# Kernel optimization log

Measured on AMD Instinct MI355X. Metric: run time of the kernel, lower is better.

The kernel has to match this reference:

```python
import jax, jax.numpy as jnp
import numpy as np

B, T, N, F = 4, 12, 768, 32
H, K, KT, L = 64, 2, 3, 2
E = 24576
EPS = 1e-5


def setup_inputs() -> dict:
    key = jax.random.key(0)
    ks = iter(jax.random.split(key, 32))
    nrm = lambda shp, s=0.05: jax.random.normal(next(ks), shp, jnp.float32) * s
    inp = dict(
        x=jax.random.normal(next(ks), (B, T, N, F), jnp.float32),
        edge_index=jax.random.randint(next(ks), (2, E), 0, N),
        edge_weight=jax.random.uniform(next(ks), (E,), jnp.float32),
        in_proj_w=nrm((F, H)), in_proj_b=jnp.zeros((H,), jnp.float32),
        tc_w=nrm((L, 2, 3, H, H, KT)),           # [layer, tconv1/2, P/Q/R, out, in, k]
        tc_b=jnp.zeros((L, 2, 3, H), jnp.float32),
        cheb_w=nrm((L, K, H, H)), cheb_b=jnp.zeros((L, H), jnp.float32),
        bn_g=jnp.ones((L, N), jnp.float32), bn_b=jnp.zeros((L, N), jnp.float32),
        ln_g=jnp.ones((L, H), jnp.float32), ln_b=jnp.zeros((L, H), jnp.float32),
        out1_w=nrm((2 * H, H // 2)), out1_b=jnp.zeros((H // 2,), jnp.float32),
        oln_g=jnp.ones((H // 2,), jnp.float32), oln_b=jnp.zeros((H // 2,), jnp.float32),
        out2_w=nrm((H // 2, 1)), out2_b=jnp.zeros((1,), jnp.float32),
    )
    return inp


def _tconv(x, w, b):
    # gated temporal conv (GLU-style), 'same' padding along T. x: [B,T,N,C]
    xt = x.transpose(0, 3, 2, 1)  # [B,C,N,T]
    pad = (KT - 1) // 2
    def c(i):
        y = jax.lax.conv_general_dilated(
            xt, w[i][:, :, None, :], (1, 1), ((0, 0), (pad, pad)),
            dimension_numbers=('NCHW', 'OIHW', 'NCHW'))
        return y + b[i][None, :, None, None]
    out = jax.nn.relu(c(0) * jax.nn.sigmoid(c(1)) + c(2))
    return out.transpose(0, 3, 2, 1)


def _cheb(x, row, col, lap_w, theta, bias):
    # ChebConv with lambda_max=2: L_hat = -D^-1/2 A D^-1/2. x: [B,T,N,C]
    def lhat(z):
        zn = z.transpose(2, 0, 1, 3)                      # [N,B,T,C]
        msg = zn[col] * lap_w[:, None, None, None]        # gather source nodes
        agg = jax.ops.segment_sum(msg, row, num_segments=N)
        return agg.transpose(1, 2, 0, 3)
    tx0 = x
    out = jnp.einsum('btnc,cd->btnd', tx0, theta[0])
    if K > 1:
        tx1 = lhat(tx0)
        out = out + jnp.einsum('btnc,cd->btnd', tx1, theta[1])
        for k in range(2, K):
            tx2 = 2.0 * lhat(tx1) - tx0
            out = out + jnp.einsum('btnc,cd->btnd', tx2, theta[k])
            tx0, tx1 = tx1, tx2
    return out + bias


def reference(x, edge_index, edge_weight, in_proj_w, in_proj_b, tc_w, tc_b,
              cheb_w, cheb_b, bn_g, bn_b, ln_g, ln_b,
              out1_w, out1_b, oln_g, oln_b, out2_w, out2_b):
    row, col = edge_index[0], edge_index[1]
    deg = jax.ops.segment_sum(edge_weight, row, num_segments=N)
    dinv = jnp.where(deg > 0, jax.lax.rsqrt(jnp.maximum(deg, 1e-12)), 0.0)
    lap_w = -dinv[row] * edge_weight * dinv[col]

    h = x @ in_proj_w + in_proj_b  # [B,T,N,H]
    for l in range(L):
        z = _tconv(h, tc_w[l, 0], tc_b[l, 0])
        z = jax.nn.relu(_cheb(z, row, col, lap_w, cheb_w[l], cheb_b[l]))
        z = _tconv(z, tc_w[l, 1], tc_b[l, 1])
        # BatchNorm2d with nodes as channels: stats over (B,T,C) per node
        mu = z.mean(axis=(0, 1, 3), keepdims=True)
        var = z.var(axis=(0, 1, 3), keepdims=True)
        z = (z - mu) * jax.lax.rsqrt(var + EPS)
        z = z * bn_g[l][None, None, :, None] + bn_b[l][None, None, :, None]
        # LayerNorm over feature dim
        m2 = z.mean(-1, keepdims=True)
        v2 = z.var(-1, keepdims=True)
        z = (z - m2) * jax.lax.rsqrt(v2 + EPS) * ln_g[l] + ln_b[l]
        h = h + z  # dropout = identity (eval)

    emb = h[:, -1]  # [B,N,H] last timestep
    # pairwise linear: cat([row_h, col_h]) @ W == row_h @ W[:H] + col_h @ W[H:]
    a = emb @ out1_w[:H]             # [B,N,H/2]
    c = emb @ out1_w[H:] + out1_b    # [B,N,H/2]
    p = jax.nn.relu(a[:, :, None, :] + c[:, None, :, :])  # [B,N,N,H/2]
    pm = p.mean(-1, keepdims=True)
    pv = p.var(-1, keepdims=True)
    p = (p - pm) * jax.lax.rsqrt(pv + EPS) * oln_g + oln_b
    logits = (p @ out2_w)[..., 0] + out2_b[0]
    return jax.nn.sigmoid(logits)  # [B,N,N]
```

## Files before the change

kernel.cpp:

```cpp
#include <hip/hip_runtime.h>
#include <math.h>

#define NODES 768
#define BB 4
#define TT 12
#define FF 32
#define HH 64
#define EE 24576
#define EPSV 1e-5f

typedef short bf16x8 __attribute__((ext_vector_type(8)));
typedef float f32x4  __attribute__((ext_vector_type(4)));

__device__ __forceinline__ unsigned short f2bf(float f) {
  union { float f; unsigned int u; } c; c.f = f;
  unsigned int u = c.u;
  unsigned int r = (u + 0x7FFFu + ((u >> 16) & 1u)) >> 16;
  return (unsigned short)r;
}

constexpr int OFF_ROWPTR = 1600;
constexpr int OFF_COLS   = 3200;
constexpr int OFF_WSEW   = 27776;
constexpr int OFF_WT     = 52352;
constexpr int OFF_THT    = 199808;
constexpr int OFF_WIN    = 216192;
constexpr int OFF_GW     = 222336;
constexpr int OFF_H      = 222400;
constexpr int OFF_ZA     = 2581696;
constexpr int OFF_ZB     = 4940992;
constexpr int OFF_AGG    = 7300288;
constexpr int OFF_A      = 9661120;
constexpr int OFF_C      = 9759424;

__global__ void prep_kernel(const float* __restrict__ tc_w, const float* __restrict__ cheb_w,
                            const float* __restrict__ in_proj_w, const float* __restrict__ out1_w,
                            const float* __restrict__ oln_g, const float* __restrict__ oln_b,
                            const float* __restrict__ out2_w, float* __restrict__ ws) {
  int idx = blockIdx.x * 256 + threadIdx.x;
  if (idx < 147456) {
    int lj = idx / 36864; int r = idx % 36864;
    int ks = r / 6144;    int r2 = r % 6144;
    int nt = r2 / 512;    int r3 = r2 % 512;
    int l  = r3 >> 3;     int j  = r3 & 7;
    int k  = ks * 32 + ((l >> 4) << 3) + j;
    int kk = k >> 6;      int in = k & 63;
    int col = nt * 16 + (l & 15);
    int g = col >> 6;     int o  = col & 63;
    float v = tc_w[(((lj * 3 + g) * 64 + o) * 64 + in) * 3 + kk];
    ((unsigned short*)(ws + OFF_WT))[idx] = f2bf(v);
  }
  int idx2 = idx - 147456;
  if (idx2 >= 0 && idx2 < 16384) {
    int i = idx2 & 63; int t = idx2 >> 6;
    int o = t & 63; t >>= 6;
    int k = t & 1; int l = t >> 1;
    ws[OFF_THT + idx2] = cheb_w[((l*2 + k)*64 + i)*64 + o];
  }
  int idx3 = idx2 - 16384;
  if (idx3 >= 0 && idx3 < 2048) {
    int i = idx3 & 31; int o = idx3 >> 5;
    ws[OFF_WIN + idx3] = in_proj_w[i*64 + o];
  }
  int idx6 = idx3 - 2048;
  if (idx6 == 0) {
    float S1 = 0.f, S2 = 0.f;
    for (int d = 0; d < 32; d++) {
      float gw = oln_g[d] * out2_w[d];
      ws[OFF_GW + d] = gw;
      S1 += gw;
      S2 += oln_b[d] * out2_w[d];
    }
    ws[OFF_GW + 32] = S1;
    ws[OFF_GW + 33] = S2;
  }
}

__global__ __launch_bounds__(1024) void graph_kernel(const int* __restrict__ ei,
                                                     const float* __restrict__ ew,
                                                     float* __restrict__ ws) {
  __shared__ float sdeg[NODES];
  __shared__ int scnt[NODES];
  __shared__ int soff[NODES];
  __shared__ int sscan[NODES];
  int tid = threadIdx.x;
  if (tid < NODES) { sdeg[tid] = 0.f; scnt[tid] = 0; }
  __syncthreads();
  for (int e = tid; e < EE; e += 1024) {
    int r = ei[e];
    atomicAdd(&sdeg[r], ew[e]);
    atomicAdd(&scnt[r], 1);
  }
  __syncthreads();
  int c = (tid < NODES) ? scnt[tid] : 0;
  if (tid < NODES) sscan[tid] = c;
  __syncthreads();
  for (int d = 1; d < NODES; d <<= 1) {
    int v = 0;
    if (tid < NODES && tid >= d) v = sscan[tid - d];
    __syncthreads();
    if (tid < NODES) sscan[tid] += v;
    __syncthreads();
  }
  if (tid < NODES) {
    soff[tid] = sscan[tid] - c;
    ((int*)ws)[OFF_ROWPTR + tid + 1] = sscan[tid];
    if (tid == 0) ((int*)ws)[OFF_ROWPTR] = 0;
  }
  __syncthreads();
  for (int e = tid; e < EE; e += 1024) {
    int r = ei[e];
    int col = ei[EE + e];
    float w = ew[e];
    float dr = sdeg[r], dc = sdeg[col];
    float dir = dr > 0.f ? rsqrtf(fmaxf(dr, 1e-12f)) : 0.f;
    float dic = dc > 0.f ? rsqrtf(fmaxf(dc, 1e-12f)) : 0.f;
    float lw = -dir * w * dic;
    int pos = atomicAdd(&soff[r], 1);
    ((int*)ws)[OFF_COLS + pos] = col;
    ws[OFF_WSEW + pos] = lw;
  }
}

__global__ __launch_bounds__(64) void inproj_kernel(const float* __restrict__ x,
                                                    const float* __restrict__ in_proj_b,
                                                    float* __restrict__ ws) {
  int bid = blockIdx.x;
  int r0 = (bid >> 2) << 6;
  int o0 = (bid & 3) << 4;
  int row = r0 + threadIdx.x;
  float xr[32];
  const float4* xp = (const float4*)(x + row * 32);
#pragma unroll
  for (int i = 0; i < 8; i++) {
    float4 v = xp[i];
    xr[4*i] = v.x; xr[4*i+1] = v.y; xr[4*i+2] = v.z; xr[4*i+3] = v.w;
  }
  const float* WT = ws + OFF_WIN;
  float* h = ws + OFF_H;
  float4 res[4];
  float* rf = (float*)res;
#pragma unroll
  for (int oo = 0; oo < 16; oo++) {
    int o = o0 + oo;
    float acc = in_proj_b[o];
#pragma unroll
    for (int i = 0; i < 32; i++) acc += xr[i] * WT[o * 32 + i];
    rf[oo] = acc;
  }
  float4* op = (float4*)(h + row * 64 + o0);
#pragma unroll
  for (int q = 0; q < 4; q++) op[q] = res[q];
}

__global__ __launch_bounds__(256) void tconv_kernel(const float* __restrict__ src,
                                                    float* __restrict__ dst,
                                                    const unsigned short* __restrict__ WB,
                                                    const float* __restrict__ bias) {
  __shared__ unsigned short zls[3072];
  __shared__ float cbuf[12 * 192];
  unsigned char* zb = (unsigned char*)zls;
  int tid = threadIdx.x;
  int lane = tid & 63;
  int w = tid >> 6;
  int P0 = blockIdx.x * 3;
  int b  = P0 / NODES;
  int n0 = P0 % NODES;

  bf16x8 bfr[6][3];
#pragma unroll
  for (int ks = 0; ks < 6; ks++) {
#pragma unroll
    for (int c = 0; c < 3; c++) {
      int nt = w * 3 + c;
      bfr[ks][c] = *(const bf16x8*)(WB + (((ks * 12 + nt) * 64 + lane) << 3));
    }
  }
  float B0 = bias[tid & 63];
  float B1 = bias[64 + (tid & 63)];
  float B2 = bias[128 + (tid & 63)];

  for (int e = tid; e < 384; e += 256) {
    int pl = e / 128; int rr = (e >> 6) & 1; int in = e & 63;
    int ts = rr ? 13 : 0;
    int off = pl * 1792 + ts * 128 + ((in * 2) ^ ((ts & 7) << 4));
    *(unsigned short*)(zb + off) = 0;
  }
  for (int e = tid; e < 576; e += 256) {
    int pl = e / 192; int rem = e % 192; int t = rem >> 4; int i4 = rem & 15;
    int c0 = i4 << 2;
    float4 v = *(const float4*)(src + ((b * TT + t) * NODES + n0 + pl) * HH + c0);
    int ts = t + 1;
    int base = pl * 1792 + ts * 128;
    unsigned int lo = ((unsigned int)f2bf(v.y) << 16) | f2bf(v.x);
    unsigned int hi = ((unsigned int)f2bf(v.w) << 16) | f2bf(v.z);
    *(unsigned int*)(zb + (base + (((c0    ) * 2) ^ ((ts & 7) << 4)))) = lo;
    *(unsigned int*)(zb + (base + (((c0 + 2) * 2) ^ ((ts & 7) << 4)))) = hi;
  }
  __syncthreads();

  int tb = (lane >> 4) << 2;
  int cc = lane & 15;
  for (int p = 0; p < 3; p++) {
    bf16x8 afr[6];
#pragma unroll
    for (int ks = 0; ks < 6; ks++) {
      int k0 = ks * 32 + ((lane >> 4) << 3);
      int kk = k0 >> 6; int in0 = k0 & 63;
      int ts = (lane & 15) + kk;
      int off = p * 1792 + ts * 128 + ((in0 * 2) ^ ((ts & 7) << 4));
      afr[ks] = *(const bf16x8*)(zb + off);
    }
    f32x4 a0 = {0.f, 0.f, 0.f, 0.f};
    f32x4 a1 = a0, a2 = a0;
#pragma unroll
    for (int ks = 0; ks < 6; ks++) {
      a0 = __builtin_amdgcn_mfma_f32_16x16x32_bf16(afr[ks], bfr[ks][0], a0, 0, 0, 0);
      a1 = __builtin_amdgcn_mfma_f32_16x16x32_bf16(afr[ks], bfr[ks][1], a1, 0, 0, 0);
      a2 = __builtin_amdgcn_mfma_f32_16x16x32_bf16(afr[ks], bfr[ks][2], a2, 0, 0, 0);
    }
    __syncthreads();
#pragma unroll
    for (int r = 0; r < 4; r++) {
      int t = tb + r;
      if (t < 12) {
        cbuf[t * 192 + (w * 3 + 0) * 16 + cc] = a0[r];
        cbuf[t * 192 + (w * 3 + 1) * 16 + cc] = a1[r];
        cbuf[t * 192 + (w * 3 + 2) * 16 + cc] = a2[r];
      }
    }
    __syncthreads();
    int o = tid & 63;
    int n = n0 + p;
#pragma unroll
    for (int m = 0; m < 3; m++) {
      int t = (tid >> 6) + (m << 2);
      float v0 = cbuf[t * 192 + o]       + B0;
      float v1 = cbuf[t * 192 + 64 + o]  + B1;
      float v2 = cbuf[t * 192 + 128 + o] + B2;
      float g = 1.f / (1.f + __expf(-v1));
      dst[((b * TT + t) * NODES + n) * HH + o] = fmaxf(v0 * g + v2, 0.f);
    }
  }
}

__global__ __launch_bounds__(256) void agg_kernel(const float* __restrict__ za,
                                                  float* __restrict__ agg,
                                                  const float* __restrict__ ws) {
  int n = blockIdx.x >> 1;
  int half = blockIdx.x & 1;
  const int* rowptr = (const int*)ws + OFF_ROWPTR;
  const int* cols = (const int*)ws + OFF_COLS;
  const float* wsrt = ws + OFF_WSEW;
  int e0 = rowptr[n], e1 = rowptr[n + 1];
  int tid = threadIdx.x;
  int hh = tid & 63;
  int bt0 = tid >> 6;
  float acc[6];
#pragma unroll
  for (int p = 0; p < 6; p++) acc[p] = 0.f;
  for (int e = e0; e < e1; e++) {
    int c = cols[e];
    float w = wsrt[e];
    const float* zp = za + c * HH + hh;
#pragma unroll
    for (int p = 0; p < 6; p++) {
      int bt = bt0 + (((half * 6) + p) << 2);
      acc[p] += w * zp[bt * NODES * HH];
    }
  }
#pragma unroll
  for (int p = 0; p < 6; p++) {
    int bt = bt0 + (((half * 6) + p) << 2);
    agg[(bt * NODES + n) * HH + hh] = acc[p];
  }
}

__global__ __launch_bounds__(64) void cheb_kernel(const float* __restrict__ za,
                                                  const float* __restrict__ agg,
                                                  float* __restrict__ zb,
                                                  const float* __restrict__ thetaT,
                                                  const float* __restrict__ bias) {
  int bid = blockIdx.x;
  int r0 = (bid >> 2) << 6;
  int o0 = (bid & 3) << 4;
  int row = r0 + threadIdx.x;
  float xz[64], xa[64];
  const float4* zp = (const float4*)(za + row * 64);
  const float4* ap = (const float4*)(agg + row * 64);
#pragma unroll
  for (int i = 0; i < 16; i++) {
    float4 v = zp[i];
    xz[4*i] = v.x; xz[4*i+1] = v.y; xz[4*i+2] = v.z; xz[4*i+3] = v.w;
    float4 w = ap[i];
    xa[4*i] = w.x; xa[4*i+1] = w.y; xa[4*i+2] = w.z; xa[4*i+3] = w.w;
  }
  float4 res[4];
  float* rf = (float*)res;
#pragma unroll
  for (int oo = 0; oo < 16; oo++) {
    int o = o0 + oo;
    float acc = bias[o];
    const float* t0 = thetaT + o * 64;
    const float* t1 = thetaT + 4096 + o * 64;
#pragma unroll
    for (int i = 0; i < 64; i++) acc += xz[i] * t0[i] + xa[i] * t1[i];
    rf[oo] = fmaxf(acc, 0.f);
  }
  float4* op = (float4*)(zb + row * 64 + o0);
#pragma unroll
  for (int q = 0; q < 4; q++) op[q] = res[q];
}

__global__ __launch_bounds__(256) void bn_kernel(const float* __restrict__ z,
                                                 float* __restrict__ h,
                                                 const float* __restrict__ bn_g,
                                                 const float* __restrict__ bn_b,
                                                 const float* __restrict__ ln_g,
                                                 const float* __restrict__ ln_b) {
  __shared__ float zl[48 * 64];
  __shared__ float rs[4], rss[4];
  __shared__ float sstat[2];
  int n = blockIdx.x;
  int tid = threadIdx.x;
  int wave = tid >> 6, lane = tid & 63;
  float s = 0.f, ss = 0.f;
  for (int p = tid; p < 3072; p += 256) {
    int bt = p >> 6, hh = p & 63;
    float v = z[(bt * NODES + n) * HH + hh];
    zl[p] = v;
    s += v; ss += v * v;
  }
#pragma unroll
  for (int d = 32; d >= 1; d >>= 1) { s += __shfl_down(s, d, 64); ss += __shfl_down(ss, d, 64); }
  if (lane == 0) { rs[wave] = s; rss[wave] = ss; }
  __syncthreads();
  if (tid == 0) {
    float S = rs[0] + rs[1] + rs[2] + rs[3];
    float SS = rss[0] + rss[1] + rss[2] + rss[3];
    float m = S / 3072.f;
    float var = SS / 3072.f - m * m;
    sstat[0] = m; sstat[1] = rsqrtf(var + EPSV);
  }
  __syncthreads();
  float mu = sstat[0], rstd = sstat[1];
  float bg = bn_g[n] * rstd;
  float bbb = bn_b[n] - mu * bg;
  float lg = ln_g[lane], lb = ln_b[lane];
  for (int k = 0; k < 12; k++) {
    int bt = wave + (k << 2);
    float v = zl[bt * 64 + lane] * bg + bbb;
    float s1 = v, s2 = v * v;
#pragma unroll
    for (int d = 32; d >= 1; d >>= 1) { s1 += __shfl_xor(s1, d, 64); s2 += __shfl_xor(s2, d, 64); }
    float m = s1 * (1.f / 64.f);
    float var = s2 * (1.f / 64.f) - m * m;
    float r2 = rsqrtf(var + EPSV);
    v = (v - m) * r2 * lg + lb;
    h[(bt * NODES + n) * HH + lane] += v;
  }
}

__global__ __launch_bounds__(256) void proj_kernel(const float* __restrict__ out1_w,
                                                   const float* __restrict__ out1_b,
                                                   float* __restrict__ ws) {
  __shared__ float wl[128 * 32];
  __shared__ float rl[4][64];
  int r0 = blockIdx.x * 4;
  int tid = threadIdx.x;
  const float* h = ws + OFF_H;
  for (int p = tid; p < 4096; p += 256) wl[p] = out1_w[p];
  {
    int rr = tid >> 6, ii = tid & 63;
    int row = r0 + rr;
    int b = row / NODES, n = row % NODES;
    rl[rr][ii] = h[((b * TT + (TT - 1)) * NODES + n) * 64 + ii];
  }
  __syncthreads();
  int rr = tid >> 6;
  int o = tid & 63;
  int part = o >> 5, oc = o & 31;
  float acc = part ? out1_b[oc] : 0.f;
  const float* wcol = wl + part * 64 * 32;
#pragma unroll
  for (int i = 0; i < 64; i++) acc += rl[rr][i] * wcol[i * 32 + oc];
  int row = r0 + rr;
  if (part == 0) (ws + OFF_A)[row * 32 + oc] = acc;
  else           (ws + OFF_C)[row * 32 + oc] = acc;
}

__global__ __launch_bounds__(256) void pair_kernel(const float* __restrict__ ws,
                                                   const float* __restrict__ out2_b,
                                                   float* __restrict__ out) {
  __shared__ float al[16 * 33], cl[16 * 33], gwl[34];
  int bidx = blockIdx.x;
  int b = bidx / (48 * 48);
  int rem = bidx % (48 * 48);
  int i0 = (rem / 48) * 16;
  int j0 = (rem % 48) * 16;
  int tid = threadIdx.x;
  const float* abuf = ws + OFF_A;
  const float* cbuf = ws + OFF_C;
  if (tid < 34) gwl[tid] = ws[OFF_GW + tid];
  for (int p = tid; p < 512; p += 256) {
    int rr = p >> 5, dd = p & 31;
    al[rr * 33 + dd] = abuf[(b * NODES + i0 + rr) * 32 + dd];
    cl[rr * 33 + dd] = cbuf[(b * NODES + j0 + rr) * 32 + dd];
  }
  __syncthreads();
  int ti = tid >> 4;
  int tj = tid & 15;
  float s1 = 0.f, s2 = 0.f, sg = 0.f;
#pragma unroll
  for (int d = 0; d < 32; d++) {
    float v = al[ti * 33 + d] + cl[tj * 33 + d];
    v = fmaxf(v, 0.f);
    s1 += v; s2 += v * v; sg += v * gwl[d];
  }
  float m = s1 * (1.f / 32.f);
  float var = s2 * (1.f / 32.f) - m * m;
  float rstd = rsqrtf(var + EPSV);
  float logit = rstd * (sg - m * gwl[32]) + gwl[33] + out2_b[0];
  float sig = 1.f / (1.f + __expf(-logit));
  out[(b * NODES + (i0 + ti)) * NODES + (j0 + tj)] = sig;
}

extern "C" void kernel_launch(void* const* d_in, const int* in_sizes, int n_in,
                              void* d_out, int out_size, void* d_ws, size_t ws_size,
                              hipStream_t stream) {
  const float* x          = (const float*)d_in[0];
  const int*   edge_index = (const int*)d_in[1];
  const float* edge_weight= (const float*)d_in[2];
  const float* in_proj_w  = (const float*)d_in[3];
  const float* in_proj_b  = (const float*)d_in[4];
  const float* tc_w       = (const float*)d_in[5];
  const float* tc_b       = (const float*)d_in[6];
  const float* cheb_w     = (const float*)d_in[7];
  const float* cheb_b     = (const float*)d_in[8];
  const float* bn_g       = (const float*)d_in[9];
  const float* bn_b       = (const float*)d_in[10];
  const float* ln_g       = (const float*)d_in[11];
  const float* ln_b       = (const float*)d_in[12];
  const float* out1_w     = (const float*)d_in[13];
  const float* out1_b     = (const float*)d_in[14];
  const float* oln_g      = (const float*)d_in[15];
  const float* oln_b      = (const float*)d_in[16];
  const float* out2_w     = (const float*)d_in[17];
  const float* out2_b     = (const float*)d_in[18];
  float* ws  = (float*)d_ws;
  float* out = (float*)d_out;

  hipLaunchKernelGGL(prep_kernel, dim3(668), dim3(256), 0, stream,
                     tc_w, cheb_w, in_proj_w, out1_w, oln_g, oln_b, out2_w, ws);
  hipLaunchKernelGGL(graph_kernel, dim3(1), dim3(1024), 0, stream, edge_index, edge_weight, ws);
  hipLaunchKernelGGL(inproj_kernel, dim3(2304), dim3(64), 0, stream, x, in_proj_b, ws);

  float* h   = ws + OFF_H;
  float* za  = ws + OFF_ZA;
  float* zb  = ws + OFF_ZB;
  float* agg = ws + OFF_AGG;
  const unsigned short* WB = (const unsigned short*)(ws + OFF_WT);

  for (int l = 0; l < 2; l++) {
    hipLaunchKernelGGL(tconv_kernel, dim3(1024), dim3(256), 0, stream,
                       h, za, WB + (l * 2 + 0) * 36864, tc_b + (l * 2 + 0) * 192);
    hipLaunchKernelGGL(agg_kernel, dim3(1536), dim3(256), 0, stream, za, agg, ws);
    hipLaunchKernelGGL(cheb_kernel, dim3(2304), dim3(64), 0, stream,
                       za, agg, zb, ws + OFF_THT + l * 8192, cheb_b + l * 64);
    hipLaunchKernelGGL(tconv_kernel, dim3(1024), dim3(256), 0, stream,
                       zb, za, WB + (l * 2 + 1) * 36864, tc_b + (l * 2 + 1) * 192);
    hipLaunchKernelGGL(bn_kernel, dim3(768), dim3(256), 0, stream,
                       za, h, bn_g + l * NODES, bn_b + l * NODES,
                       ln_g + l * 64, ln_b + l * 64);
  }

  hipLaunchKernelGGL(proj_kernel, dim3(768), dim3(256), 0, stream, out1_w, out1_b, ws);
  hipLaunchKernelGGL(pair_kernel, dim3(9216), dim3(256), 0, stream, ws, out2_b, out);
}
```

Measured before the change: 377.9 us.

## Split single-block graph build into parallel count, scan, and scatter kernels

Replaces the one-block graph_kernel, which did degree counting, prefix scan and CSR scatter with 1024 threads, with three kernels. Counting and scatter now run across 96 blocks using global atomics, and a single 768-thread block does the scan. The aim is to spread the serial edge work over many CUs. The cost is two extra launches and global rather than shared-memory atomics. Degree and count buffers are zeroed in prep_kernel.

```diff
diff --git a/kernel.cpp b/kernel.cpp
--- a/kernel.cpp
+++ b/kernel.cpp
@@ -19,7 +19,10 @@
   return (unsigned short)r;
 }
 
+constexpr int OFF_DEG    = 0;
+constexpr int OFF_CNT    = 768;
 constexpr int OFF_ROWPTR = 1600;
+constexpr int OFF_OFF    = 2432;
 constexpr int OFF_COLS   = 3200;
 constexpr int OFF_WSEW   = 27776;
 constexpr int OFF_WT     = 52352;
@@ -62,7 +65,12 @@
     int i = idx3 & 31; int o = idx3 >> 5;
     ws[OFF_WIN + idx3] = in_proj_w[i*64 + o];
   }
-  int idx6 = idx3 - 2048;
+  int idx5 = idx3 - 2048;
+  if (idx5 >= 0 && idx5 < 768) {
+    ws[OFF_DEG + idx5] = 0.0f;
+    ((int*)ws)[OFF_CNT + idx5] = 0;
+  }
+  int idx6 = idx5 - 768;
   if (idx6 == 0) {
     float S1 = 0.f, S2 = 0.f;
     for (int d = 0; d < 32; d++) {
@@ -76,50 +84,49 @@
   }
 }
 
-__global__ __launch_bounds__(1024) void graph_kernel(const int* __restrict__ ei,
-                                                     const float* __restrict__ ew,
-                                                     float* __restrict__ ws) {
-  __shared__ float sdeg[NODES];
-  __shared__ int scnt[NODES];
-  __shared__ int soff[NODES];
-  __shared__ int sscan[NODES];
-  int tid = threadIdx.x;
-  if (tid < NODES) { sdeg[tid] = 0.f; scnt[tid] = 0; }
-  __syncthreads();
-  for (int e = tid; e < EE; e += 1024) {
-    int r = ei[e];
-    atomicAdd(&sdeg[r], ew[e]);
-    atomicAdd(&scnt[r], 1);
-  }
-  __syncthreads();
-  int c = (tid < NODES) ? scnt[tid] : 0;
-  if (tid < NODES) sscan[tid] = c;
+__global__ void count_kernel(const int* __restrict__ edge_index, const float* __restrict__ ew,
+                             float* __restrict__ ws) {
+  int e = blockIdx.x * 256 + threadIdx.x;
+  if (e >= EE) return;
+  int r = edge_index[e];
+  atomicAdd(&ws[OFF_DEG + r], ew[e]);
+  atomicAdd(&((int*)ws)[OFF_CNT + r], 1);
+}
+
+__global__ void scan_kernel(float* __restrict__ ws) {
+  __shared__ int s[NODES];
+  int t = threadIdx.x;
+  int* counts = (int*)ws + OFF_CNT;
+  int* rowptr = (int*)ws + OFF_ROWPTR;
+  int* off    = (int*)ws + OFF_OFF;
+  int c = counts[t];
+  s[t] = c;
   __syncthreads();
   for (int d = 1; d < NODES; d <<= 1) {
-    int v = 0;
-    if (tid < NODES && tid >= d) v = sscan[tid - d];
+    int v = (t >= d) ? s[t - d] : 0;
     __syncthreads();
-    if (tid < NODES) sscan[tid] += v;
+    s[t] += v;
     __syncthreads();
   }
-  if (tid < NODES) {
-    soff[tid] = sscan[tid] - c;
-    ((int*)ws)[OFF_ROWPTR + tid + 1] = sscan[tid];
-    if (tid == 0) ((int*)ws)[OFF_ROWPTR] = 0;
-  }
-  __syncthreads();
-  for (int e = tid; e < EE; e += 1024) {
-    int r = ei[e];
-    int col = ei[EE + e];
-    float w = ew[e];
-    float dr = sdeg[r], dc = sdeg[col];
-    float dir = dr > 0.f ? rsqrtf(fmaxf(dr, 1e-12f)) : 0.f;
-    float dic = dc > 0.f ? rsqrtf(fmaxf(dc, 1e-12f)) : 0.f;
-    float lw = -dir * w * dic;
-    int pos = atomicAdd(&soff[r], 1);
-    ((int*)ws)[OFF_COLS + pos] = col;
-    ws[OFF_WSEW + pos] = lw;
-  }
+  rowptr[t + 1] = s[t];
+  if (t == 0) rowptr[0] = 0;
+  off[t] = s[t] - c;
+}
+
+__global__ void scatter_kernel(const int* __restrict__ edge_index, const float* __restrict__ ew,
+                               float* __restrict__ ws) {
+  int e = blockIdx.x * 256 + threadIdx.x;
+  if (e >= EE) return;
+  int r = edge_index[e];
+  int c = edge_index[EE + e];
+  float w = ew[e];
+  float dr = ws[OFF_DEG + r], dc = ws[OFF_DEG + c];
+  float dir = dr > 0.f ? rsqrtf(fmaxf(dr, 1e-12f)) : 0.f;
+  float dic = dc > 0.f ? rsqrtf(fmaxf(dc, 1e-12f)) : 0.f;
+  float lw = -dir * w * dic;
+  int pos = atomicAdd(&((int*)ws)[OFF_OFF + r], 1);
+  ((int*)ws)[OFF_COLS + pos] = c;
+  ws[OFF_WSEW + pos] = lw;
 }
 
 __global__ __launch_bounds__(64) void inproj_kernel(const float* __restrict__ x,
@@ -452,7 +459,9 @@
 
   hipLaunchKernelGGL(prep_kernel, dim3(668), dim3(256), 0, stream,
                      tc_w, cheb_w, in_proj_w, out1_w, oln_g, oln_b, out2_w, ws);
-  hipLaunchKernelGGL(graph_kernel, dim3(1), dim3(1024), 0, stream, edge_index, edge_weight, ws);
+  hipLaunchKernelGGL(count_kernel, dim3(96), dim3(256), 0, stream, edge_index, edge_weight, ws);
+  hipLaunchKernelGGL(scan_kernel, dim3(1), dim3(768), 0, stream, ws);
+  hipLaunchKernelGGL(scatter_kernel, dim3(96), dim3(256), 0, stream, edge_index, edge_weight, ws);
   hipLaunchKernelGGL(inproj_kernel, dim3(2304), dim3(64), 0, stream, x, in_proj_b, ws);
 
   float* h   = ws + OFF_H;
```

After: 321.6 us. -14.9%, faster.
